# Kernel tuning notes

Measured on AMD Instinct MI355X. Metric: run time of the kernel, lower is better.

Reference implementation:

```python
import jax, jax.numpy as jnp
import numpy as np

N = 100000   # nodes
E = 3200000  # edges (avg degree 32)
D = 128      # in_channels
H = 128      # hidden_channels
A, S, ETH = 3, 2, 3  # head output dims


def _w(k, o, i):
    return jax.random.normal(k, (o, i), dtype=jnp.float32) / np.sqrt(i).astype(np.float32)


def setup_inputs() -> dict:
    key = jax.random.key(0)
    ks = jax.random.split(key, 20)
    x = jax.random.normal(ks[0], (N, D), dtype=jnp.float32)
    edge_index = jax.random.randint(ks[1], (2, E), 0, N, dtype=jnp.int64)
    inp = {"x": x, "edge_index": edge_index}
    # SAGEConv params: Wl applied to mean-aggregated neighbors, Wr to root, plus bias
    dims = [("1", D, H), ("2", H, H), ("3", H, H), ("a", H, A), ("s", H, S), ("e", H, ETH)]
    ki = 2
    for tag, i, o in dims:
        inp[f"W{tag}l"] = _w(ks[ki], o, i); ki += 1
        inp[f"W{tag}r"] = _w(ks[ki], o, i); ki += 1
        inp[f"b{tag}"] = jnp.zeros((o,), dtype=jnp.float32)
    return inp


def _sage(x, src, dst, inv_deg, Wl, Wr, b):
    # mean aggregation of source features onto destination nodes, then linear
    agg = jax.ops.segment_sum(x[src], dst, num_segments=N) * inv_deg  # [N, d]
    return agg @ Wl.T + x @ Wr.T + b


def reference(x, edge_index,
              W1l, W1r, b1, W2l, W2r, b2, W3l, W3r, b3,
              Wal, War, ba, Wsl, Wsr, bs, Wel, Wer, be):
    src, dst = edge_index[0], edge_index[1]
    deg = jax.ops.segment_sum(jnp.ones((E,), jnp.float32), dst, num_segments=N)
    inv_deg = (1.0 / jnp.maximum(deg, 1.0))[:, None]  # [N,1]
    h = jax.nn.relu(_sage(x, src, dst, inv_deg, W1l, W1r, b1))
    h = jax.nn.relu(_sage(h, src, dst, inv_deg, W2l, W2r, b2))
    h = jax.nn.relu(_sage(h, src, dst, inv_deg, W3l, W3r, b3))
    age_out = _sage(h, src, dst, inv_deg, Wal, War, ba)
    sex_out = _sage(h, src, dst, inv_deg, Wsl, Wsr, bs)
    eth_out = _sage(h, src, dst, inv_deg, Wel, Wer, be)
    return (age_out, sex_out, eth_out)
```

## Files before the change

### kernel.cpp

```cpp
#include <hip/hip_runtime.h>

#define TPB 256
#define NB1 256
#define NBUCK 512

using half4_t = __attribute__((ext_vector_type(4))) _Float16;
using half8_t = __attribute__((ext_vector_type(8))) _Float16;
using f32x4 = __attribute__((ext_vector_type(4))) float;


__global__ __launch_bounds__(256) void hist1_k(const int* __restrict__ ei,
                                               int* __restrict__ hist, int E, int stripe) {
  __shared__ int h[NBUCK];
  for (int i = threadIdx.x; i < NBUCK; i += 256) h[i] = 0;
  __syncthreads();
  int b0 = blockIdx.x * stripe;
  int b1 = min(b0 + stripe, E);
  for (int e = b0 + threadIdx.x; e < b1; e += 256) atomicAdd(&h[ei[E + e] >> 8], 1);
  __syncthreads();
  for (int i = threadIdx.x; i < NBUCK; i += 256) hist[i * NB1 + blockIdx.x] = h[i];
}

__global__ void scan1_k(const int* __restrict__ src, int* __restrict__ out,
                        int* __restrict__ chunk, int n) {
  __shared__ int sh[TPB];
  int i = blockIdx.x * TPB + threadIdx.x;
  int v = (i < n) ? src[i] : 0;
  sh[threadIdx.x] = v;
  __syncthreads();
  for (int off = 1; off < TPB; off <<= 1) {
    int t = (threadIdx.x >= off) ? sh[threadIdx.x - off] : 0;
    __syncthreads();
    sh[threadIdx.x] += t;
    __syncthreads();
  }
  if (i < n) out[i] = sh[threadIdx.x] - v;
  if (threadIdx.x == TPB - 1) chunk[blockIdx.x] = sh[TPB - 1];
}

__global__ void scan2_k(int* __restrict__ chunk, int nb) {
  __shared__ int sh[512];
  int v = (threadIdx.x < nb) ? chunk[threadIdx.x] : 0;
  sh[threadIdx.x] = v;
  __syncthreads();
  for (int off = 1; off < 512; off <<= 1) {
    int t = (threadIdx.x >= off) ? sh[threadIdx.x - off] : 0;
    __syncthreads();
    sh[threadIdx.x] += t;
    __syncthreads();
  }
  if (threadIdx.x < nb) chunk[threadIdx.x] = sh[threadIdx.x] - v;
}

__global__ void scan3_k(int* __restrict__ out, const int* __restrict__ chunk, int n) {
  int i = blockIdx.x * TPB + threadIdx.x;
  if (i < n) out[i] += chunk[blockIdx.x];
}

__global__ __launch_bounds__(256) void scatter1_k(const int* __restrict__ ei,
                                                  const int* __restrict__ base,
                                                  unsigned* __restrict__ ebuf, int E,
                                                  int stripe) {
  __shared__ int cur[NBUCK];
  for (int i = threadIdx.x; i < NBUCK; i += 256) cur[i] = base[i * NB1 + blockIdx.x];
  __syncthreads();
  int b0 = blockIdx.x * stripe;
  int b1 = min(b0 + stripe, E);
  for (int e = b0 + threadIdx.x; e < b1; e += 256) {
    int s = ei[e];
    int d = ei[E + e];
    int p = atomicAdd(&cur[d >> 8], 1);
    ebuf[p] = (unsigned)s | ((unsigned)(d & 255) << 24);
  }
}

__global__ __launch_bounds__(256) void build_k(const unsigned* __restrict__ ebuf,
                                               const int* __restrict__ base,
                                               int* __restrict__ row_start,
                                               int* __restrict__ deg,
                                               float* __restrict__ invd,
                                               int* __restrict__ csr, int N, int E) {
  __shared__ int h[256];
  __shared__ int excl[256];
  __shared__ int bse[2];
  int b = blockIdx.x;
  int t = threadIdx.x;
  if (t == 0) {
    bse[0] = base[b * NB1];
    bse[1] = (b + 1 < NBUCK) ? base[(b + 1) * NB1] : E;
  }
  h[t] = 0;
  __syncthreads();
  int bs = bse[0], be = bse[1];
  for (int e = bs + t; e < be; e += 256) atomicAdd(&h[ebuf[e] >> 24], 1);
  __syncthreads();
  int v = h[t];
  excl[t] = v;
  __syncthreads();
  for (int off = 1; off < 256; off <<= 1) {
    int tv = (t >= off) ? excl[t - off] : 0;
    __syncthreads();
    excl[t] += tv;
    __syncthreads();
  }
  int ex = excl[t] - v;
  int node = b * 256 + t;
  if (node < N) {
    row_start[node] = bs + ex;
    deg[node] = v;
    invd[node] = 1.0f / fmaxf((float)v, 1.0f);
  }
  h[t] = bs + ex;
  __syncthreads();
  for (int e = bs + t; e < be; e += 256) {
    unsigned p = ebuf[e];
    int pos = atomicAdd(&h[p >> 24], 1);
    csr[pos] = (int)(p & 0xFFFFFFu);
  }
}


__global__ void f2h_k(const float* __restrict__ in, _Float16* __restrict__ out, int n4) {
  int i = blockIdx.x * TPB + threadIdx.x;
  if (i < n4) {
    float4 v = ((const float4*)in)[i];
    half4_t o;
    o.x = (_Float16)v.x; o.y = (_Float16)v.y; o.z = (_Float16)v.z; o.w = (_Float16)v.w;
    ((half4_t*)out)[i] = o;
  }
}

__global__ void w6_k(const float* __restrict__ w0, const float* __restrict__ w1,
                     const float* __restrict__ w2, const float* __restrict__ w3,
                     const float* __restrict__ w4, const float* __restrict__ w5,
                     _Float16* __restrict__ out) {
  int t = blockIdx.x * TPB + threadIdx.x;
  if (t >= 6 * 4096) return;
  int which = t >> 12, i = t & 4095;
  const float* src = which == 0 ? w0 : which == 1 ? w1 : which == 2 ? w2
                   : which == 3 ? w3 : which == 4 ? w4 : w5;
  float4 v = ((const float4*)src)[i];
  half4_t o;
  o.x = (_Float16)v.x; o.y = (_Float16)v.y; o.z = (_Float16)v.z; o.w = (_Float16)v.w;
  ((half4_t*)out)[(size_t)which * 4096 + i] = o;
}


__global__ void pack_head_k(const float* __restrict__ Wal, const float* __restrict__ War,
                            const float* __restrict__ ba, const float* __restrict__ Wsl,
                            const float* __restrict__ Wsr, const float* __restrict__ bsx,
                            const float* __restrict__ Wel, const float* __restrict__ Wer,
                            const float* __restrict__ be, _Float16* __restrict__ Wcat,
                            float* __restrict__ bcat) {
  int t = blockIdx.x * TPB + threadIdx.x;
  float v = 0.f;
  bool ok = t < 2048;
  if (t < 384) v = Wal[t];
  else if (t < 640) v = Wsl[t - 384];
  else if (t < 1024) v = Wel[t - 640];
  else if (t < 1408) v = War[t - 1024];
  else if (t < 1664) v = Wsr[t - 1408];
  else if (t < 2048) v = Wer[t - 1664];
  if (ok) Wcat[t] = (_Float16)v;
  if (t < 16) {
    float b = 0.f;
    if (t >= 8 && t < 11) b = ba[t - 8];
    else if (t >= 11 && t < 13) b = bsx[t - 11];
    else if (t >= 13) b = be[t - 13];
    bcat[t] = b;
  }
}


__global__ __launch_bounds__(256) void fused_sage_k(
    const _Float16* __restrict__ hin, const _Float16* __restrict__ Wh,
    const float* __restrict__ bias, const int* __restrict__ csr,
    const int* __restrict__ row_start, const int* __restrict__ deg,
    const float* __restrict__ invd, _Float16* __restrict__ hout,
    const _Float16* __restrict__ Wcat, const float* __restrict__ bcat,
    float* __restrict__ head_out, int n, int mode) {
  __shared__ _Float16 At[64][144];
  int wave = threadIdx.x >> 6;
  int lane = threadIdx.x & 63;
  int g = lane >> 4;
  int l = lane & 15;
  int ms = blockIdx.x * 64 + wave * 16;

  const _Float16* gbase = hin + (l << 3);
  for (int i = 0; i < 16; ++i) {
    int node = ms + i;
    float a0 = 0.f, a1 = 0.f, a2 = 0.f, a3 = 0.f;
    float a4 = 0.f, a5 = 0.f, a6 = 0.f, a7 = 0.f;
    if (node < n) {
      int s = row_start[node];
      int c = deg[node];
      int j = 0;
      if (c >= 16) {
        int id[4];
#pragma unroll
        for (int p = 0; p < 4; ++p) id[p] = csr[s + 4 * p + g];
        while (true) {
          half8_t v[4];
#pragma unroll
          for (int p = 0; p < 4; ++p) v[p] = *(const half8_t*)&gbase[(size_t)id[p] * 128];
          j += 16;
          bool more = (j + 16 <= c);
          if (more) {
#pragma unroll
            for (int p = 0; p < 4; ++p) id[p] = csr[s + j + 4 * p + g];
          }
#pragma unroll
          for (int p = 0; p < 4; ++p) {
            a0 += (float)v[p][0]; a1 += (float)v[p][1];
            a2 += (float)v[p][2]; a3 += (float)v[p][3];
            a4 += (float)v[p][4]; a5 += (float)v[p][5];
            a6 += (float)v[p][6]; a7 += (float)v[p][7];
          }
          if (!more) break;
        }
      }
      if (j < c) {
        int cm1 = c - 1;
#pragma unroll
        for (int p = 0; p < 4; ++p) {
          int e = j + 4 * p + g;
          float m = (e < c) ? 1.f : 0.f;
          int id = csr[s + min(e, cm1)];
          half8_t v = *(const half8_t*)&gbase[(size_t)id * 128];
          a0 = fmaf(m, (float)v[0], a0); a1 = fmaf(m, (float)v[1], a1);
          a2 = fmaf(m, (float)v[2], a2); a3 = fmaf(m, (float)v[3], a3);
          a4 = fmaf(m, (float)v[4], a4); a5 = fmaf(m, (float)v[5], a5);
          a6 = fmaf(m, (float)v[6], a6); a7 = fmaf(m, (float)v[7], a7);
        }
      }
    }
    a0 += __shfl_xor(a0, 16); a1 += __shfl_xor(a1, 16);
    a2 += __shfl_xor(a2, 16); a3 += __shfl_xor(a3, 16);
    a4 += __shfl_xor(a4, 16); a5 += __shfl_xor(a5, 16);
    a6 += __shfl_xor(a6, 16); a7 += __shfl_xor(a7, 16);
    a0 += __shfl_xor(a0, 32); a1 += __shfl_xor(a1, 32);
    a2 += __shfl_xor(a2, 32); a3 += __shfl_xor(a3, 32);
    a4 += __shfl_xor(a4, 32); a5 += __shfl_xor(a5, 32);
    a6 += __shfl_xor(a6, 32); a7 += __shfl_xor(a7, 32);
    if (g == 0) {
      float w = (node < n) ? invd[node] : 0.f;
      half8_t r;
      r[0] = (_Float16)(a0 * w); r[1] = (_Float16)(a1 * w);
      r[2] = (_Float16)(a2 * w); r[3] = (_Float16)(a3 * w);
      r[4] = (_Float16)(a4 * w); r[5] = (_Float16)(a5 * w);
      r[6] = (_Float16)(a6 * w); r[7] = (_Float16)(a7 * w);
      *(half8_t*)&At[wave * 16 + i][l << 3] = r;
    }
  }
  __syncthreads();

  int arow = ms + l;
  bool valid = arow < n;
  f32x4 acc[8];
#pragma unroll
  for (int c = 0; c < 8; ++c) acc[c] = (f32x4){0.f, 0.f, 0.f, 0.f};

#pragma unroll
  for (int kb = 0; kb < 128; kb += 32) {
    half8_t af = *(const half8_t*)&At[wave * 16 + l][kb + g * 8];
#pragma unroll
    for (int c = 0; c < 8; ++c) {
      half8_t bf = *(const half8_t*)&Wh[(size_t)(c * 16 + l) * 128 + kb + g * 8];
      acc[c] = __builtin_amdgcn_mfma_f32_16x16x32_f16(af, bf, acc[c], 0, 0, 0);
    }
  }
  {
    const _Float16* W2 = Wh + 16384;
    size_t abase = (size_t)arow * 128 + g * 8;
#pragma unroll
    for (int kb = 0; kb < 128; kb += 32) {
      half8_t af;
      if (valid) {
        af = *(const half8_t*)&hin[abase + kb];
      } else {
#pragma unroll
        for (int jj = 0; jj < 8; ++jj) af[jj] = (_Float16)0;
      }
#pragma unroll
      for (int c = 0; c < 8; ++c) {
        half8_t bf = *(const half8_t*)&W2[(size_t)(c * 16 + l) * 128 + kb + g * 8];
        acc[c] = __builtin_amdgcn_mfma_f32_16x16x32_f16(af, bf, acc[c], 0, 0, 0);
      }
    }
  }

  if (mode == 0) {
#pragma unroll
    for (int c = 0; c < 8; ++c) {
      float bcol = bias[c * 16 + l];
#pragma unroll
      for (int r = 0; r < 4; ++r) {
        int row = ms + g * 4 + r;
        if (row < n) {
          float v = fmaxf(acc[c][r] + bcol, 0.f);
          hout[(size_t)row * 128 + c * 16 + l] = (_Float16)v;
        }
      }
    }
  } else {
    __syncthreads();
#pragma unroll
    for (int c = 0; c < 8; ++c) {
      float bcol = bias[c * 16 + l];
#pragma unroll
      for (int r = 0; r < 4; ++r) {
        float v = fmaxf(acc[c][r] + bcol, 0.f);
        At[wave * 16 + g * 4 + r][c * 16 + l] = (_Float16)v;
      }
    }
    __syncthreads();
    f32x4 ah = (f32x4){0.f, 0.f, 0.f, 0.f};
#pragma unroll
    for (int kb = 0; kb < 128; kb += 32) {
      half8_t af = *(const half8_t*)&At[wave * 16 + l][kb + g * 8];
      half8_t bf = *(const half8_t*)&Wcat[(size_t)l * 128 + kb + g * 8];
      ah = __builtin_amdgcn_mfma_f32_16x16x32_f16(af, bf, ah, 0, 0, 0);
    }
    float bcol = bcat[l];
#pragma unroll
    for (int r = 0; r < 4; ++r) {
      int row = ms + g * 4 + r;
      if (row < n) head_out[(size_t)row * 16 + l] = ah[r] + bcol;
    }
  }
}


__global__ void agg8_k(const float* __restrict__ hlr, const int* __restrict__ csr,
                       const int* __restrict__ row_start, const int* __restrict__ deg,
                       const float* __restrict__ invd, float* __restrict__ out, int n) {
  int node = (blockIdx.x << 2) + (threadIdx.x >> 6);
  if (node >= n) return;
  int lane = threadIdx.x & 63;
  int c2 = lane & 3;
  int g = lane >> 2;
  int s = row_start[node], cnt = deg[node];
  float ax = 0.f, ay = 0.f;
  int j = 0;
  for (; j + 32 <= cnt; j += 32) {
#pragma unroll
    for (int p = 0; p < 2; ++p) {
      int id = csr[s + j + 16 * p + g];
      float2 v = *(const float2*)&hlr[(size_t)id * 16 + 2 * c2];
      ax += v.x;
      ay += v.y;
    }
  }
  if (j < cnt) {
    int cm1 = cnt - 1;
#pragma unroll
    for (int p = 0; p < 2; ++p) {
      int e = j + 16 * p + g;
      float m = (e < cnt) ? 1.f : 0.f;
      int id = csr[s + min(e, cm1)];
      float2 v = *(const float2*)&hlr[(size_t)id * 16 + 2 * c2];
      ax = fmaf(m, v.x, ax);
      ay = fmaf(m, v.y, ay);
    }
  }
  ax += __shfl_xor(ax, 4);  ay += __shfl_xor(ay, 4);
  ax += __shfl_xor(ax, 8);  ay += __shfl_xor(ay, 8);
  ax += __shfl_xor(ax, 16); ay += __shfl_xor(ay, 16);
  ax += __shfl_xor(ax, 32); ay += __shfl_xor(ay, 32);
  if (g == 0) {
    float w = invd[node];
    float r0 = ax * w + hlr[(size_t)node * 16 + 8 + 2 * c2];
    float r1 = ay * w + hlr[(size_t)node * 16 + 8 + 2 * c2 + 1];
    float rr[2] = {r0, r1};
#pragma unroll
    for (int q = 0; q < 2; ++q) {
      int f = 2 * c2 + q;
      float r = rr[q];
      if (f < 3) out[(size_t)node * 3 + f] = r;
      else if (f < 5) out[(size_t)3 * n + (size_t)node * 2 + (f - 3)] = r;
      else out[(size_t)5 * n + (size_t)node * 3 + (f - 5)] = r;
    }
  }
}


extern "C" void kernel_launch(void* const* d_in, const int* in_sizes, int n_in,
                              void* d_out, int out_size, void* d_ws, size_t ws_size,
                              hipStream_t stream) {
  const float* x = (const float*)d_in[0];
  const int* ei = (const int*)d_in[1];
  const float* W1l = (const float*)d_in[2];
  const float* W1r = (const float*)d_in[3];
  const float* b1 = (const float*)d_in[4];
  const float* W2l = (const float*)d_in[5];
  const float* W2r = (const float*)d_in[6];
  const float* b2 = (const float*)d_in[7];
  const float* W3l = (const float*)d_in[8];
  const float* W3r = (const float*)d_in[9];
  const float* b3 = (const float*)d_in[10];
  const float* Wal = (const float*)d_in[11];
  const float* War = (const float*)d_in[12];
  const float* ba = (const float*)d_in[13];
  const float* Wsl = (const float*)d_in[14];
  const float* Wsr = (const float*)d_in[15];
  const float* bsx = (const float*)d_in[16];
  const float* Wel = (const float*)d_in[17];
  const float* Wer = (const float*)d_in[18];
  const float* be = (const float*)d_in[19];

  int N = in_sizes[0] / 128;
  int E = in_sizes[1] / 2;
  int NBKT = (N + 255) >> 8;

  char* w = (char*)d_ws;
  auto alloc = [&](size_t b) {
    char* p = w;
    w += (b + 255) & ~(size_t)255;
    return p;
  };
  int* deg = (int*)alloc((size_t)N * 4);
  int* row_start = (int*)alloc((size_t)N * 4);
  float* invd = (float*)alloc((size_t)N * 4);
  int* hist = (int*)alloc((size_t)NBUCK * NB1 * 4);
  int* chunk = (int*)alloc(512 * 4);
  int* csr = (int*)alloc((size_t)E * 4);
  size_t xh_bytes = (size_t)N * 128 * 2;
  size_t ebuf_bytes = (size_t)E * 4;
  char* region = (char*)alloc(xh_bytes > ebuf_bytes ? xh_bytes : ebuf_bytes);
  unsigned* ebuf = (unsigned*)region;
  _Float16* xh = (_Float16*)region;
  _Float16* hA = (_Float16*)alloc((size_t)N * 128 * 2);
  _Float16* hB = (_Float16*)alloc((size_t)N * 128 * 2);
  _Float16* wh = (_Float16*)alloc((size_t)6 * 16384 * 2);
  _Float16* Wcat = (_Float16*)alloc(2048 * 2);
  float* bcat = (float*)alloc(16 * 4);
  float* head_lr = (float*)alloc((size_t)N * 16 * 4);

  int stripe = (((E + NB1 - 1) / NB1) + 255) & ~255;
  int nscan = NBUCK * NB1;
  int nbScan = (nscan + TPB - 1) / TPB;
  int nbNode = (N + 3) / 4;
  int nbM = (N + 63) / 64;
  int nbC = (N * 32 + TPB - 1) / TPB;

  hist1_k<<<NB1, 256, 0, stream>>>(ei, hist, E, stripe);
  scan1_k<<<nbScan, TPB, 0, stream>>>(hist, hist, chunk, nscan);
  scan2_k<<<1, 512, 0, stream>>>(chunk, nbScan);
  scan3_k<<<nbScan, TPB, 0, stream>>>(hist, chunk, nscan);
  scatter1_k<<<NB1, 256, 0, stream>>>(ei, hist, ebuf, E, stripe);
  build_k<<<NBKT, 256, 0, stream>>>(ebuf, hist, row_start, deg, invd, csr, N, E);

  f2h_k<<<nbC, TPB, 0, stream>>>(x, xh, N * 32);
  w6_k<<<96, TPB, 0, stream>>>(W1l, W1r, W2l, W2r, W3l, W3r, wh);
  pack_head_k<<<8, TPB, 0, stream>>>(Wal, War, ba, Wsl, Wsr, bsx, Wel, Wer, be, Wcat, bcat);

  fused_sage_k<<<nbM, TPB, 0, stream>>>(xh, wh + 0 * 16384, b1, csr, row_start, deg,
                                        invd, hA, nullptr, nullptr, nullptr, N, 0);
  fused_sage_k<<<nbM, TPB, 0, stream>>>(hA, wh + 2 * 16384, b2, csr, row_start, deg,
                                        invd, hB, nullptr, nullptr, nullptr, N, 0);
  fused_sage_k<<<nbM, TPB, 0, stream>>>(hB, wh + 4 * 16384, b3, csr, row_start, deg,
                                        invd, nullptr, Wcat, bcat, head_lr, N, 1);
  agg8_k<<<nbNode, TPB, 0, stream>>>(head_lr, csr, row_start, deg, invd, (float*)d_out, N);
}
```

Measured before the change: 782.3 us.

## Shrink fused SAGE tile to 16 nodes per block, split output columns across waves

Each block now handles 16 nodes instead of 64. Each wave gathers 4 nodes and computes 32 output columns of the shared 16-row tile, rather than owning 16 rows and all 128 columns. Row starts and degrees for the wave's 4 nodes are loaded up front, and the next node's first CSR indices are prefetched while the current node accumulates, which hides index latency. The goal is more blocks, better load balance and fewer accumulator registers. In exchange, each block reloads the weight matrix four times as often, and in head mode only one wave does the final head MFMA.

Result: faster. 688.4 us (-12.0%).

```diff
diff --git a/kernel.cpp b/kernel.cpp
--- a/kernel.cpp
+++ b/kernel.cpp
@@ -179,59 +179,73 @@
     const float* __restrict__ invd, _Float16* __restrict__ hout,
     const _Float16* __restrict__ Wcat, const float* __restrict__ bcat,
     float* __restrict__ head_out, int n, int mode) {
-  __shared__ _Float16 At[64][144];
+  __shared__ _Float16 At[16][144];
   int wave = threadIdx.x >> 6;
   int lane = threadIdx.x & 63;
   int g = lane >> 4;
   int l = lane & 15;
-  int ms = blockIdx.x * 64 + wave * 16;
+  int ms = blockIdx.x * 16;
 
   const _Float16* gbase = hin + (l << 3);
-  for (int i = 0; i < 16; ++i) {
-    int node = ms + i;
+  int nb = ms + wave * 4;
+  int rs[4], dg[4];
+#pragma unroll
+  for (int i = 0; i < 4; ++i) {
+    int nd = nb + i;
+    bool ok = nd < n;
+    rs[i] = ok ? row_start[nd] : 0;
+    dg[i] = ok ? deg[nd] : 0;
+  }
+  int nid[4];
+  if (dg[0] >= 16) {
+#pragma unroll
+    for (int p = 0; p < 4; ++p) nid[p] = csr[rs[0] + 4 * p + g];
+  }
+  for (int i = 0; i < 4; ++i) {
+    int s = rs[i], c = dg[i];
     float a0 = 0.f, a1 = 0.f, a2 = 0.f, a3 = 0.f;
     float a4 = 0.f, a5 = 0.f, a6 = 0.f, a7 = 0.f;
-    if (node < n) {
-      int s = row_start[node];
-      int c = deg[node];
-      int j = 0;
-      if (c >= 16) {
-        int id[4];
-#pragma unroll
-        for (int p = 0; p < 4; ++p) id[p] = csr[s + 4 * p + g];
-        while (true) {
-          half8_t v[4];
-#pragma unroll
-          for (int p = 0; p < 4; ++p) v[p] = *(const half8_t*)&gbase[(size_t)id[p] * 128];
-          j += 16;
-          bool more = (j + 16 <= c);
-          if (more) {
-#pragma unroll
-            for (int p = 0; p < 4; ++p) id[p] = csr[s + j + 4 * p + g];
-          }
-#pragma unroll
-          for (int p = 0; p < 4; ++p) {
-            a0 += (float)v[p][0]; a1 += (float)v[p][1];
-            a2 += (float)v[p][2]; a3 += (float)v[p][3];
-            a4 += (float)v[p][4]; a5 += (float)v[p][5];
-            a6 += (float)v[p][6]; a7 += (float)v[p][7];
-          }
-          if (!more) break;
+    int j = 0;
+    if (c >= 16) {
+      int id[4];
+#pragma unroll
+      for (int p = 0; p < 4; ++p) id[p] = nid[p];
+      while (true) {
+        half8_t v[4];
+#pragma unroll
+        for (int p = 0; p < 4; ++p) v[p] = *(const half8_t*)&gbase[(size_t)id[p] * 128];
+        j += 16;
+        bool more = (j + 16 <= c);
+        if (more) {
+#pragma unroll
+          for (int p = 0; p < 4; ++p) id[p] = csr[s + j + 4 * p + g];
         }
-      }
-      if (j < c) {
-        int cm1 = c - 1;
 #pragma unroll
         for (int p = 0; p < 4; ++p) {
-          int e = j + 4 * p + g;
-          float m = (e < c) ? 1.f : 0.f;
-          int id = csr[s + min(e, cm1)];
-          half8_t v = *(const half8_t*)&gbase[(size_t)id * 128];
-          a0 = fmaf(m, (float)v[0], a0); a1 = fmaf(m, (float)v[1], a1);
-          a2 = fmaf(m, (float)v[2], a2); a3 = fmaf(m, (float)v[3], a3);
-          a4 = fmaf(m, (float)v[4], a4); a5 = fmaf(m, (float)v[5], a5);
-          a6 = fmaf(m, (float)v[6], a6); a7 = fmaf(m, (float)v[7], a7);
+          a0 += (float)v[p][0]; a1 += (float)v[p][1];
+          a2 += (float)v[p][2]; a3 += (float)v[p][3];
+          a4 += (float)v[p][4]; a5 += (float)v[p][5];
+          a6 += (float)v[p][6]; a7 += (float)v[p][7];
         }
+        if (!more) break;
+      }
+    }
+    if (i < 3 && dg[i + 1] >= 16) {
+#pragma unroll
+      for (int p = 0; p < 4; ++p) nid[p] = csr[rs[i + 1] + 4 * p + g];
+    }
+    if (j < c) {
+      int cm1 = c - 1;
+#pragma unroll
+      for (int p = 0; p < 4; ++p) {
+        int e = j + 4 * p + g;
+        float m = (e < c) ? 1.f : 0.f;
+        int id = csr[s + min(e, cm1)];
+        half8_t v = *(const half8_t*)&gbase[(size_t)id * 128];
+        a0 = fmaf(m, (float)v[0], a0); a1 = fmaf(m, (float)v[1], a1);
+        a2 = fmaf(m, (float)v[2], a2); a3 = fmaf(m, (float)v[3], a3);
+        a4 = fmaf(m, (float)v[4], a4); a5 = fmaf(m, (float)v[5], a5);
+        a6 = fmaf(m, (float)v[6], a6); a7 = fmaf(m, (float)v[7], a7);
       }
     }
     a0 += __shfl_xor(a0, 16); a1 += __shfl_xor(a1, 16);
@@ -243,30 +257,32 @@
     a4 += __shfl_xor(a4, 32); a5 += __shfl_xor(a5, 32);
     a6 += __shfl_xor(a6, 32); a7 += __shfl_xor(a7, 32);
     if (g == 0) {
+      int node = nb + i;
       float w = (node < n) ? invd[node] : 0.f;
       half8_t r;
       r[0] = (_Float16)(a0 * w); r[1] = (_Float16)(a1 * w);
       r[2] = (_Float16)(a2 * w); r[3] = (_Float16)(a3 * w);
       r[4] = (_Float16)(a4 * w); r[5] = (_Float16)(a5 * w);
       r[6] = (_Float16)(a6 * w); r[7] = (_Float16)(a7 * w);
-      *(half8_t*)&At[wave * 16 + i][l << 3] = r;
+      *(half8_t*)&At[wave * 4 + i][l << 3] = r;
     }
   }
   __syncthreads();
 
   int arow = ms + l;
   bool valid = arow < n;
-  f32x4 acc[8];
-#pragma unroll
-  for (int c = 0; c < 8; ++c) acc[c] = (f32x4){0.f, 0.f, 0.f, 0.f};
+  f32x4 acc[2];
+  acc[0] = (f32x4){0.f, 0.f, 0.f, 0.f};
+  acc[1] = (f32x4){0.f, 0.f, 0.f, 0.f};
 
 #pragma unroll
   for (int kb = 0; kb < 128; kb += 32) {
-    half8_t af = *(const half8_t*)&At[wave * 16 + l][kb + g * 8];
-#pragma unroll
-    for (int c = 0; c < 8; ++c) {
-      half8_t bf = *(const half8_t*)&Wh[(size_t)(c * 16 + l) * 128 + kb + g * 8];
-      acc[c] = __builtin_amdgcn_mfma_f32_16x16x32_f16(af, bf, acc[c], 0, 0, 0);
+    half8_t af = *(const half8_t*)&At[l][kb + g * 8];
+#pragma unroll
+    for (int ct = 0; ct < 2; ++ct) {
+      int ocol = wave * 32 + ct * 16 + l;
+      half8_t bf = *(const half8_t*)&Wh[(size_t)ocol * 128 + kb + g * 8];
+      acc[ct] = __builtin_amdgcn_mfma_f32_16x16x32_f16(af, bf, acc[ct], 0, 0, 0);
     }
   }
   {
@@ -282,50 +298,55 @@
         for (int jj = 0; jj < 8; ++jj) af[jj] = (_Float16)0;
       }
 #pragma unroll
-      for (int c = 0; c < 8; ++c) {
-        half8_t bf = *(const half8_t*)&W2[(size_t)(c * 16 + l) * 128 + kb + g * 8];
-        acc[c] = __builtin_amdgcn_mfma_f32_16x16x32_f16(af, bf, acc[c], 0, 0, 0);
+      for (int ct = 0; ct < 2; ++ct) {
+        int ocol = wave * 32 + ct * 16 + l;
+        half8_t bf = *(const half8_t*)&W2[(size_t)ocol * 128 + kb + g * 8];
+        acc[ct] = __builtin_amdgcn_mfma_f32_16x16x32_f16(af, bf, acc[ct], 0, 0, 0);
       }
     }
   }
 
   if (mode == 0) {
 #pragma unroll
-    for (int c = 0; c < 8; ++c) {
-      float bcol = bias[c * 16 + l];
+    for (int ct = 0; ct < 2; ++ct) {
+      int col = wave * 32 + ct * 16 + l;
+      float bcol = bias[col];
 #pragma unroll
       for (int r = 0; r < 4; ++r) {
         int row = ms + g * 4 + r;
         if (row < n) {
-          float v = fmaxf(acc[c][r] + bcol, 0.f);
-          hout[(size_t)row * 128 + c * 16 + l] = (_Float16)v;
+          float v = fmaxf(acc[ct][r] + bcol, 0.f);
+          hout[(size_t)row * 128 + col] = (_Float16)v;
         }
       }
     }
   } else {
     __syncthreads();
 #pragma unroll
-    for (int c = 0; c < 8; ++c) {
-      float bcol = bias[c * 16 + l];
+    for (int ct = 0; ct < 2; ++ct) {
+      int col = wave * 32 + ct * 16 + l;
+      float bcol = bias[col];
 #pragma unroll
       for (int r = 0; r < 4; ++r) {
-        float v = fmaxf(acc[c][r] + bcol, 0.f);
-        At[wave * 16 + g * 4 + r][c * 16 + l] = (_Float16)v;
-      }
-    }
-    __syncthreads();
-    f32x4 ah = (f32x4){0.f, 0.f, 0.f, 0.f};
-#pragma unroll
-    for (int kb = 0; kb < 128; kb += 32) {
-      half8_t af = *(const half8_t*)&At[wave * 16 + l][kb + g * 8];
-      half8_t bf = *(const half8_t*)&Wcat[(size_t)l * 128 + kb + g * 8];
-      ah = __builtin_amdgcn_mfma_f32_16x16x32_f16(af, bf, ah, 0, 0, 0);
-    }
-    float bcol = bcat[l];
-#pragma unroll
-    for (int r = 0; r < 4; ++r) {
-      int row = ms + g * 4 + r;
-      if (row < n) head_out[(size_t)row * 16 + l] = ah[r] + bcol;
+        float v = fmaxf(acc[ct][r] + bcol, 0.f);
+        At[g * 4 + r][col] = (_Float16)v;
+      }
+    }
+    __syncthreads();
+    if (wave == 0) {
+      f32x4 ah = (f32x4){0.f, 0.f, 0.f, 0.f};
+#pragma unroll
+      for (int kb = 0; kb < 128; kb += 32) {
+        half8_t af = *(const half8_t*)&At[l][kb + g * 8];
+        half8_t bf = *(const half8_t*)&Wcat[(size_t)l * 128 + kb + g * 8];
+        ah = __builtin_amdgcn_mfma_f32_16x16x32_f16(af, bf, ah, 0, 0, 0);
+      }
+      float bcol = bcat[l];
+#pragma unroll
+      for (int r = 0; r < 4; ++r) {
+        int row = ms + g * 4 + r;
+        if (row < n) head_out[(size_t)row * 16 + l] = ah[r] + bcol;
+      }
     }
   }
 }
@@ -440,7 +461,7 @@
   int nscan = NBUCK * NB1;
   int nbScan = (nscan + TPB - 1) / TPB;
   int nbNode = (N + 3) / 4;
-  int nbM = (N + 63) / 64;
+  int nbM = (N + 15) / 16;
   int nbC = (N * 32 + TPB - 1) / TPB;
 
   hist1_k<<<NB1, 256, 0, stream>>>(ei, hist, E, stripe);
```
